# Performance work log

Hardware: AMD Instinct MI355X
Metric: run time of the kernel (lower is better)

Reference implementation:

```python
import jax, jax.numpy as jnp
import numpy as np

B, S, D, H = 32, 512, 1024, 16
DH = D // H
EPS = 1e-5
NEG = -1e9


def layer_norm(x, g, b):
    mu = jnp.mean(x, axis=-1, keepdims=True)
    var = jnp.mean(jnp.square(x - mu), axis=-1, keepdims=True)
    return (x - mu) * jax.lax.rsqrt(var + EPS) * g + b


def setup_inputs() -> dict:
    key = jax.random.key(0)
    ks = jax.random.split(key, 12)
    s = 1.0 / np.sqrt(D)
    inp = {
        "qk": jax.random.normal(ks[0], (B, S, D), jnp.float32),
        "v": jax.random.normal(ks[1], (B, S, D), jnp.float32),
        "mask": jax.random.randint(ks[2], (B, S), 0, 2).astype(jnp.int32),
        "qk_ln_g": jnp.ones((D,), jnp.float32),
        "qk_ln_b": jnp.zeros((D,), jnp.float32),
        "v_ln_g": jnp.ones((D,), jnp.float32),
        "v_ln_b": jnp.zeros((D,), jnp.float32),
        "Wq": jax.random.normal(ks[3], (D, D), jnp.float32) * s,
        "bq": jnp.zeros((D,), jnp.float32),
        "Wk": jax.random.normal(ks[4], (D, D), jnp.float32) * s,
        "bk": jnp.zeros((D,), jnp.float32),
        "Wv": jax.random.normal(ks[5], (D, D), jnp.float32) * s,
        "bv": jnp.zeros((D,), jnp.float32),
        "Wo": jax.random.normal(ks[6], (D, D), jnp.float32) * s,
        "bo": jnp.zeros((D,), jnp.float32),
    }
    return inp


def reference(qk, v, mask, qk_ln_g, qk_ln_b, v_ln_g, v_ln_b,
              Wq, bq, Wk, bk, Wv, bv, Wo, bo):
    # dual pre-norm
    qk_n = layer_norm(qk, qk_ln_g, qk_ln_b)          # [B,S,D]
    v_n = layer_norm(v, v_ln_g, v_ln_b)              # [B,S,D]
    # projections -> [B,S,H,DH]
    q = (qk_n @ Wq + bq).reshape(B, S, H, DH)
    k = (qk_n @ Wk + bk).reshape(B, S, H, DH)
    vv = (v_n @ Wv + bv).reshape(B, S, H, DH)
    # attention scores with key-padding mask
    scores = jnp.einsum("bqhd,bkhd->bhqk", q, k) / np.sqrt(DH)
    scores = jnp.where(mask[:, None, None, :] == 0, NEG, scores)
    attn = jax.nn.softmax(scores, axis=-1)           # [B,H,Sq,Sk]
    ctx = jnp.einsum("bhqk,bkhd->bqhd", attn, vv).reshape(B, S, D)
    a = ctx @ Wo + bo                                # output projection
    # residual on the normalized v (dropout is identity at eval)
    return v_n + a
```

## Files before the change

kernel.cpp:

```cpp
#include <hip/hip_runtime.h>
#include <hip/hip_bf16.h>

typedef __bf16 bf16;
typedef __bf16 bf16x2 __attribute__((ext_vector_type(2)));
typedef __bf16 bf16x4 __attribute__((ext_vector_type(4)));
typedef __bf16 bf16x8 __attribute__((ext_vector_type(8)));
typedef float f32x4 __attribute__((ext_vector_type(4)));

#define B_ 32
#define S_ 512
#define D_ 1024
#define H_ 16
#define DH_ 64
#define M_ (B_*S_)

#if __has_builtin(__builtin_amdgcn_exp2f)
#define FEXP2 __builtin_amdgcn_exp2f
#else
#define FEXP2 exp2f
#endif

__device__ __forceinline__ void async16(const void* g, void* l) {
  __builtin_amdgcn_global_load_lds(
      (const __attribute__((address_space(1))) unsigned int*)g,
      (__attribute__((address_space(3))) unsigned int*)l, 16, 0, 0);
}

__global__ __launch_bounds__(256) void ln_bf16(
    const float* __restrict__ qk, const float* __restrict__ v,
    const float* __restrict__ g1, const float* __restrict__ b1,
    const float* __restrict__ g2, const float* __restrict__ b2,
    bf16* __restrict__ o1, bf16* __restrict__ o2)
{
  int row = blockIdx.x;
  const float* src; const float* g; const float* b; bf16* o; int r;
  if (row < M_) { src=qk; g=g1; b=b1; o=o1; r=row; }
  else          { src=v;  g=g2; b=b2; o=o2; r=row-M_; }
  int t = threadIdx.x;
  float4 x = ((const float4*)(src + (size_t)r*D_))[t];
  float s  = x.x+x.y+x.z+x.w;
  float ss = x.x*x.x + x.y*x.y + x.z*x.z + x.w*x.w;
  #pragma unroll
  for (int off=32; off>=1; off>>=1) {
    s  += __shfl_xor(s,  off, 64);
    ss += __shfl_xor(ss, off, 64);
  }
  __shared__ float red[8];
  int w = t>>6, l = t&63;
  if (l==0){ red[w]=s; red[4+w]=ss; }
  __syncthreads();
  s  = red[0]+red[1]+red[2]+red[3];
  ss = red[4]+red[5]+red[6]+red[7];
  float mu  = s*(1.f/D_);
  float var = ss*(1.f/D_) - mu*mu;
  float rs  = rsqrtf(var + 1e-5f);
  float4 gg = ((const float4*)g)[t];
  float4 bb = ((const float4*)b)[t];
  bf16x4 ov;
  ov[0] = (bf16)((x.x-mu)*rs*gg.x + bb.x);
  ov[1] = (bf16)((x.y-mu)*rs*gg.y + bb.y);
  ov[2] = (bf16)((x.z-mu)*rs*gg.z + bb.z);
  ov[3] = (bf16)((x.w-mu)*rs*gg.w + bb.w);
  ((bf16x4*)(o + (size_t)r*D_))[t] = ov;
}

__global__ void wtrans(const float* __restrict__ W0, const float* __restrict__ W1,
                       const float* __restrict__ W2, const float* __restrict__ W3,
                       bf16* __restrict__ o0, bf16* __restrict__ o1,
                       bf16* __restrict__ o2, bf16* __restrict__ o3)
{
  int z = blockIdx.z;
  const float* W = z==0?W0: z==1?W1: z==2?W2: W3;
  bf16* o        = z==0?o0: z==1?o1: z==2?o2: o3;
  __shared__ float tile[32][33];
  int n0 = blockIdx.x*32, k0 = blockIdx.y*32;
  int tx = threadIdx.x, ty = threadIdx.y;
  #pragma unroll
  for (int i=0;i<4;i++) tile[ty + i*8][tx] = W[(size_t)(k0+ty+i*8)*D_ + n0+tx];
  __syncthreads();
  #pragma unroll
  for (int i=0;i<4;i++) o[(size_t)(n0+ty+i*8)*D_ + k0+tx] = (bf16)tile[tx][ty+i*8];
}

template<int MODE>
__global__ __launch_bounds__(512, 2) void gemm_bt(
    const bf16* __restrict__ A, const bf16* __restrict__ Bt,
    const float* __restrict__ bias0, const float* __restrict__ bias1,
    const bf16* __restrict__ res,
    bf16* __restrict__ out0, bf16* __restrict__ out1, float* __restrict__ outf)
{
  __shared__ bf16 A_sh[2][256*64];
  __shared__ bf16 B_sh[2][256*64];
  int t = threadIdx.x;
  int nwg  = gridDim.x * gridDim.y;
  int orig = blockIdx.y * gridDim.x + blockIdx.x;
  int qch  = nwg >> 3;
  int wg   = (orig & 7) * qch + (orig >> 3);
  int bx = wg % gridDim.x, by = wg / gridDim.x;
  int n0 = bx*256, m0 = by*256;
  int w = t>>6, l = t&63, lr = l&15, lg = (l>>4)&3;
  int wm = w>>2, wn = w&3;

  auto stage = [&](int buf, int kt){
    const bf16* Ab = A  + (size_t)m0*D_ + kt*64;
    const bf16* Bb = Bt + (size_t)n0*D_ + kt*64;
    #pragma unroll
    for (int i=0;i<4;i++){
      int c = i*512 + t;
      int row = c>>3, slot = (c&7) ^ (row&7);
      async16(Ab + (size_t)row*D_ + slot*8, &A_sh[buf][c*8]);
      async16(Bb + (size_t)row*D_ + slot*8, &B_sh[buf][c*8]);
    }
  };

  f32x4 acc[8][4];
  #pragma unroll
  for (int m=0;m<8;m++)
    #pragma unroll
    for (int n=0;n<4;n++) acc[m][n] = (f32x4){0.f,0.f,0.f,0.f};

  stage(0, 0);
  stage(1, 1);
  asm volatile("s_waitcnt vmcnt(8)" ::: "memory");
  __builtin_amdgcn_s_barrier();

  for (int kt=0; kt<16; ++kt) {
    int cur = kt & 1;
    bf16x8 bfr[4][2];
    #pragma unroll
    for (int n=0;n<4;n++){
      int row = wn*64 + n*16 + lr;
      #pragma unroll
      for (int kk=0;kk<2;kk++)
        bfr[n][kk] = *(const bf16x8*)&B_sh[cur][row*64 + (((kk*4+lg)^(lr&7))*8)];
    }
    __builtin_amdgcn_s_setprio(1);
    #pragma unroll
    for (int m=0;m<8;m++){
      int row = wm*128 + m*16 + lr;
      bf16x8 af0 = *(const bf16x8*)&A_sh[cur][row*64 + (((0*4+lg)^(lr&7))*8)];
      bf16x8 af1 = *(const bf16x8*)&A_sh[cur][row*64 + (((1*4+lg)^(lr&7))*8)];
      #pragma unroll
      for (int n=0;n<4;n++)
        acc[m][n] = __builtin_amdgcn_mfma_f32_16x16x32_bf16(af0, bfr[n][0], acc[m][n], 0,0,0);
      #pragma unroll
      for (int n=0;n<4;n++)
        acc[m][n] = __builtin_amdgcn_mfma_f32_16x16x32_bf16(af1, bfr[n][1], acc[m][n], 0,0,0);
    }
    __builtin_amdgcn_s_setprio(0);
    asm volatile("s_waitcnt lgkmcnt(0)" ::: "memory");
    __builtin_amdgcn_sched_barrier(0);
    __builtin_amdgcn_s_barrier();
    if (kt+2 < 16) stage(cur, kt+2);
    if (kt < 14)       asm volatile("s_waitcnt vmcnt(8)" ::: "memory");
    else if (kt == 14) asm volatile("s_waitcnt vmcnt(0)" ::: "memory");
    if (kt < 15) { __builtin_amdgcn_sched_barrier(0); __builtin_amdgcn_s_barrier(); }
  }

  if (MODE == 0) {
    #pragma unroll
    for (int n=0;n<4;n++){
      int col = n0 + wn*64 + n*16 + lr;
      bf16* dst; int c;
      if (col < D_) { dst = out0; c = col; } else { dst = out1; c = col - D_; }
      float bv = (col < D_) ? bias0[c] : bias1[c];
      #pragma unroll
      for (int m=0;m<8;m++){
        #pragma unroll
        for (int j=0;j<4;j++){
          size_t row = (size_t)m0 + wm*128 + m*16 + lg*4 + j;
          dst[row*D_ + c] = (bf16)(acc[m][n][j] + bv);
        }
      }
    }
  } else if (MODE == 1) {
    #pragma unroll
    for (int n=0;n<4;n++){
      int col = n0 + wn*64 + n*16 + lr;
      int hh = col >> 6, dh = col & 63;
      int nd = dh >> 4, lrk = dh & 15;
      float bv = bias0[col];
      #pragma unroll
      for (int m=0;m<8;m++){
        int row = m0 + wm*128 + m*16 + lg*4;
        int bb = row >> 9, sl = row & 511;
        int kt = sl >> 6, l0 = sl & 63;
        int kk = (l0>>5)&1, h8 = (l0>>4)&1, lgk = (l0>>2)&3;
        int c  = ((nd*2+kk)*4+lgk)*16 + lrk;
        bf16x4 pk4;
        #pragma unroll
        for (int j=0;j<4;j++) pk4[j] = (bf16)(acc[m][n][j] + bv);
        *(bf16x4*)&out0[(size_t)(((bb*H_ + hh)*8 + kt)*4096) + c*8 + h8*4] = pk4;
      }
    }
  } else {
    #pragma unroll
    for (int m=0;m<8;m++){
      #pragma unroll
      for (int j=0;j<4;j++){
        size_t row = (size_t)m0 + wm*128 + m*16 + lg*4 + j;
        #pragma unroll
        for (int n=0;n<4;n++){
          int col = n0 + wn*64 + n*16 + lr;
          size_t idx = row*D_ + col;
          outf[idx] = acc[m][n][j] + bias0[col] + (float)res[idx];
        }
      }
    }
  }
}

__global__ __launch_bounds__(512) void attn_fwd(
    const bf16* __restrict__ Q, const bf16* __restrict__ K,
    const bf16* __restrict__ VF, const int* __restrict__ mask,
    bf16* __restrict__ ctx)
{
  int flat = blockIdx.x + (blockIdx.y<<1) + (blockIdx.z<<5);
  int work = (flat & 7)*128 + (flat >> 3);
  int qt = work & 1, h = (work>>1) & 15, b = work >> 5;
  int q0 = qt*256;
  int t = threadIdx.x, w = t>>6, l = t&63, lr = l&15, lg = (l>>4)&3;

  __shared__ bf16 K_s[2][4096];
  __shared__ bf16 V_s[2][4096];
  __shared__ float msk[512];

  const float SC = 0.125f * 1.44269504f;
  msk[t] = mask[b*S_+t] ? 0.f : -1.44269504e9f;

  size_t qbase  = ((size_t)(b*S_ + q0)*H_ + h)*DH_;
  size_t vfbase = (size_t)(b*H_ + h)*8*4096;

  auto stageKV = [&](int slot, int kt){
    size_t kb = ((size_t)(b*S_ + kt*64)*H_ + h)*DH_;
    int clr=t&15, clg=(t>>4)&3, ckk=(t>>6)&1, n16=t>>7;
    async16(K + kb + (size_t)(n16*16+clr)*D_ + ckk*32 + clg*8, &K_s[slot][t*8]);
    async16(VF + vfbase + (size_t)kt*4096 + t*8, &V_s[slot][t*8]);
  };

  bf16x8 qa[2][2];
  #pragma unroll
  for (int s=0;s<2;s++)
    #pragma unroll
    for (int kk=0;kk<2;kk++)
      qa[s][kk] = *(const bf16x8*)(Q + qbase + (size_t)(w*32 + s*16 + lr)*D_ + kk*32 + lg*8);

  stageKV(0, 0);
  stageKV(1, 1);
  asm volatile("s_waitcnt vmcnt(2) lgkmcnt(0)" ::: "memory");
  __builtin_amdgcn_s_barrier();

  f32x4 cacc[2][4];
  #pragma unroll
  for (int s=0;s<2;s++)
    #pragma unroll
    for (int n=0;n<4;n++) cacc[s][n] = (f32x4){0.f,0.f,0.f,0.f};
  float mrun[2] = {-3.0e38f, -3.0e38f};
  float lrun[2] = {0.f, 0.f};

  union UPA { unsigned u[4]; bf16x8 v; };
  UPA pa[2][2];

  for (int kt=0; kt<8; ++kt) {
    int cur = kt & 1;
    const bf16* Ks = K_s[cur];
    const bf16* Vs = V_s[cur];

    bf16x8 kf[4][2];
    #pragma unroll
    for (int n=0;n<4;n++)
      #pragma unroll
      for (int kk=0;kk<2;kk++)
        kf[n][kk] = *(const bf16x8*)&Ks[(((n*2+kk)*4+lg)*16+lr)*8];

    #pragma unroll
    for (int s=0;s<2;s++){
      float p[4][4];
      #pragma unroll
      for (int n=0;n<4;n++){
        f32x4 sa = (f32x4){0.f,0.f,0.f,0.f};
        #pragma unroll
        for (int kk=0;kk<2;kk++)
          sa = __builtin_amdgcn_mfma_f32_16x16x32_bf16(kf[n][kk], qa[s][kk], sa, 0,0,0);
        float4 mk = *(const float4*)&msk[kt*64 + n*16 + lg*4];
        p[n][0] = sa[0]*SC + mk.x;
        p[n][1] = sa[1]*SC + mk.y;
        p[n][2] = sa[2]*SC + mk.z;
        p[n][3] = sa[3]*SC + mk.w;
      }

      float pm = fmaxf(fmaxf(p[0][0],p[0][1]),fmaxf(p[0][2],p[0][3]));
      #pragma unroll
      for (int n=1;n<4;n++)
        pm = fmaxf(pm, fmaxf(fmaxf(p[n][0],p[n][1]),fmaxf(p[n][2],p[n][3])));
      pm = fmaxf(pm, __shfl_xor(pm, 16, 64));
      pm = fmaxf(pm, __shfl_xor(pm, 32, 64));

      if (__any((int)(pm - mrun[s] > 8.f))) {
        float mnew  = fmaxf(mrun[s], pm);
        float alpha = FEXP2(mrun[s] - mnew);
        mrun[s] = mnew;
        lrun[s] *= alpha;
        #pragma unroll
        for (int n=0;n<4;n++) cacc[s][n] *= alpha;
      }
      float ps = 0.f;
      #pragma unroll
      for (int n=0;n<4;n++)
        #pragma unroll
        for (int j=0;j<4;j++){ p[n][j] = FEXP2(p[n][j] - mrun[s]); ps += p[n][j]; }
      ps += __shfl_xor(ps, 16, 64);
      ps += __shfl_xor(ps, 32, 64);
      lrun[s] += ps;

      unsigned pk[4][2];
      #pragma unroll
      for (int n=0;n<4;n++)
        #pragma unroll
        for (int i=0;i<2;i++){
          union { bf16x2 v; unsigned u; } u2;
          u2.v[0] = (bf16)p[n][2*i];
          u2.v[1] = (bf16)p[n][2*i+1];
          pk[n][i] = u2.u;
        }
      #pragma unroll
      for (int kk=0;kk<2;kk++){
        pa[s][kk].u[0] = pk[2*kk  ][0];
        pa[s][kk].u[1] = pk[2*kk  ][1];
        pa[s][kk].u[2] = pk[2*kk+1][0];
        pa[s][kk].u[3] = pk[2*kk+1][1];
      }
    }

    __builtin_amdgcn_s_setprio(1);
    #pragma unroll
    for (int nd=0;nd<4;nd++){
      bf16x8 vb0 = *(const bf16x8*)&Vs[(((nd*2+0)*4+lg)*16+lr)*8];
      bf16x8 vb1 = *(const bf16x8*)&Vs[(((nd*2+1)*4+lg)*16+lr)*8];
      #pragma unroll
      for (int s=0;s<2;s++){
        cacc[s][nd] = __builtin_amdgcn_mfma_f32_16x16x32_bf16(vb0, pa[s][0].v, cacc[s][nd], 0,0,0);
        cacc[s][nd] = __builtin_amdgcn_mfma_f32_16x16x32_bf16(vb1, pa[s][1].v, cacc[s][nd], 0,0,0);
      }
    }
    __builtin_amdgcn_s_setprio(0);

    asm volatile("s_waitcnt lgkmcnt(0)" ::: "memory");
    __builtin_amdgcn_sched_barrier(0);
    __builtin_amdgcn_s_barrier();
    if (kt+2 < 8) stageKV(cur, kt+2);

    if (kt < 6)       asm volatile("s_waitcnt vmcnt(2)" ::: "memory");
    else if (kt == 6) asm volatile("s_waitcnt vmcnt(0)" ::: "memory");
    if (kt < 7) { __builtin_amdgcn_sched_barrier(0); __builtin_amdgcn_s_barrier(); }
  }

  #pragma unroll
  for (int s=0;s<2;s++){
    float rl = 1.0f / lrun[s];
    size_t obase = qbase + (size_t)(w*32 + s*16 + lr)*D_;
    #pragma unroll
    for (int nd=0;nd<4;nd++){
      bf16x4 o4;
      #pragma unroll
      for (int j=0;j<4;j++) o4[j] = (bf16)(cacc[s][nd][j]*rl);
      *(bf16x4*)&ctx[obase + nd*16 + lg*4] = o4;
    }
  }
}

extern "C" void kernel_launch(void* const* d_in, const int* in_sizes, int n_in,
                              void* d_out, int out_size, void* d_ws, size_t ws_size,
                              hipStream_t stream)
{
  (void)in_sizes; (void)n_in; (void)out_size; (void)ws_size;
  const float* qk   = (const float*)d_in[0];
  const float* v    = (const float*)d_in[1];
  const int*   mask = (const int*)  d_in[2];
  const float* qk_g = (const float*)d_in[3];
  const float* qk_b = (const float*)d_in[4];
  const float* v_g  = (const float*)d_in[5];
  const float* v_b  = (const float*)d_in[6];
  const float* Wq   = (const float*)d_in[7];
  const float* bq   = (const float*)d_in[8];
  const float* Wk   = (const float*)d_in[9];
  const float* bk   = (const float*)d_in[10];
  const float* Wv   = (const float*)d_in[11];
  const float* bv   = (const float*)d_in[12];
  const float* Wo   = (const float*)d_in[13];
  const float* bo   = (const float*)d_in[14];
  float* out = (float*)d_out;

  char* ws = (char*)d_ws;
  size_t off = 0;
  auto alloc = [&](size_t bytes){ void* p = ws + off; off += (bytes + 255) & ~(size_t)255; return p; };
  bf16* qkn  = (bf16*)alloc((size_t)M_*D_*2);
  bf16* vn   = (bf16*)alloc((size_t)M_*D_*2);
  bf16* Qb   = (bf16*)alloc((size_t)M_*D_*2);
  bf16* Kb   = (bf16*)alloc((size_t)M_*D_*2);
  bf16* VFb  = (bf16*)alloc((size_t)M_*D_*2);
  bf16* Cb   = (bf16*)alloc((size_t)M_*D_*2);
  bf16* WqkT = (bf16*)alloc((size_t)2*D_*D_*2);
  bf16* WvT  = (bf16*)alloc((size_t)D_*D_*2);
  bf16* WoT  = (bf16*)alloc((size_t)D_*D_*2);

  ln_bf16<<<2*M_, 256, 0, stream>>>(qk, v, qk_g, qk_b, v_g, v_b, qkn, vn);
  wtrans<<<dim3(32,32,4), dim3(32,8), 0, stream>>>(Wq, Wk, Wv, Wo,
      WqkT, WqkT + (size_t)D_*D_, WvT, WoT);
  gemm_bt<0><<<dim3(8,64), 512, 0, stream>>>(qkn, WqkT, bq, bk, nullptr, Qb, Kb, nullptr);
  gemm_bt<1><<<dim3(4,64), 512, 0, stream>>>(vn,  WvT,  bv, nullptr, nullptr, VFb, nullptr, nullptr);
  attn_fwd<<<dim3(2, 16, 32), 512, 0, stream>>>(Qb, Kb, VFb, mask, Cb);
  gemm_bt<2><<<dim3(4,64), 512, 0, stream>>>(Cb, WoT, bo, nullptr, vn, nullptr, nullptr, out);
}
```

Measured before the change: 274.9 us.

## Interleave split A/B tile loads with MFMA phases in GEMM main loop

Restructures the bf16 GEMM main loop into four sub-phases per k-tile. Each phase issues a half-tile async load of A (next k-tile) or B (two k-tiles ahead) between fragment reads and MFMA bursts, with a barrier per phase, so global-to-LDS traffic is spread across the compute instead of issued in one burst. It also drops the occupancy hint of 2 blocks per CU from launch bounds, which frees registers but may lower occupancy. The extra barriers and the tighter buffer reuse add synchronisation overhead and risk of LDS races.

After: 259.9 us. 5.4% less time.

```diff
diff --git a/kernel.cpp b/kernel.cpp
--- a/kernel.cpp
+++ b/kernel.cpp
@@ -83,7 +83,7 @@
 }
 
 template<int MODE>
-__global__ __launch_bounds__(512, 2) void gemm_bt(
+__global__ __launch_bounds__(512) void gemm8(
     const bf16* __restrict__ A, const bf16* __restrict__ Bt,
     const float* __restrict__ bias0, const float* __restrict__ bias1,
     const bf16* __restrict__ res,
@@ -101,17 +101,28 @@
   int w = t>>6, l = t&63, lr = l&15, lg = (l>>4)&3;
   int wm = w>>2, wn = w&3;
 
-  auto stage = [&](int buf, int kt){
-    const bf16* Ab = A  + (size_t)m0*D_ + kt*64;
-    const bf16* Bb = Bt + (size_t)n0*D_ + kt*64;
-    #pragma unroll
-    for (int i=0;i<4;i++){
+  auto stageA = [&](int kt, int half){
+    if (kt >= 16) return;
+    int buf = kt & 1;
+    const bf16* Ab = A + (size_t)(m0 + half*128)*D_ + kt*64;
+    #pragma unroll
+    for (int i=0;i<2;i++){
       int c = i*512 + t;
       int row = c>>3, slot = (c&7) ^ (row&7);
-      async16(Ab + (size_t)row*D_ + slot*8, &A_sh[buf][c*8]);
-      async16(Bb + (size_t)row*D_ + slot*8, &B_sh[buf][c*8]);
+      async16(Ab + (size_t)row*D_ + slot*8, &A_sh[buf][(half*1024 + c)*8]);
     }
   };
+  auto stageB = [&](int kt, int half){
+    if (kt >= 16) return;
+    int buf = kt & 1;
+    const bf16* Bb = Bt + (size_t)(n0 + half*128)*D_ + kt*64;
+    #pragma unroll
+    for (int i=0;i<2;i++){
+      int c = i*512 + t;
+      int row = c>>3, slot = (c&7) ^ (row&7);
+      async16(Bb + (size_t)row*D_ + slot*8, &B_sh[buf][(half*1024 + c)*8]);
+    }
+  };
 
   f32x4 acc[8][4];
   #pragma unroll
@@ -119,42 +130,60 @@
     #pragma unroll
     for (int n=0;n<4;n++) acc[m][n] = (f32x4){0.f,0.f,0.f,0.f};
 
-  stage(0, 0);
-  stage(1, 1);
-  asm volatile("s_waitcnt vmcnt(8)" ::: "memory");
+  stageA(0,0); stageA(0,1); stageB(0,0); stageB(0,1);
+  stageB(1,0); stageB(1,1);
+  asm volatile("s_waitcnt vmcnt(4)" ::: "memory");
   __builtin_amdgcn_s_barrier();
 
-  for (int kt=0; kt<16; ++kt) {
-    int cur = kt & 1;
-    bf16x8 bfr[4][2];
-    #pragma unroll
-    for (int n=0;n<4;n++){
-      int row = wn*64 + n*16 + lr;
-      #pragma unroll
-      for (int kk=0;kk<2;kk++)
-        bfr[n][kk] = *(const bf16x8*)&B_sh[cur][row*64 + (((kk*4+lg)^(lr&7))*8)];
-    }
-    __builtin_amdgcn_s_setprio(1);
-    #pragma unroll
-    for (int m=0;m<8;m++){
-      int row = wm*128 + m*16 + lr;
-      bf16x8 af0 = *(const bf16x8*)&A_sh[cur][row*64 + (((0*4+lg)^(lr&7))*8)];
-      bf16x8 af1 = *(const bf16x8*)&A_sh[cur][row*64 + (((1*4+lg)^(lr&7))*8)];
-      #pragma unroll
-      for (int n=0;n<4;n++)
-        acc[m][n] = __builtin_amdgcn_mfma_f32_16x16x32_bf16(af0, bfr[n][0], acc[m][n], 0,0,0);
-      #pragma unroll
-      for (int n=0;n<4;n++)
-        acc[m][n] = __builtin_amdgcn_mfma_f32_16x16x32_bf16(af1, bfr[n][1], acc[m][n], 0,0,0);
-    }
-    __builtin_amdgcn_s_setprio(0);
-    asm volatile("s_waitcnt lgkmcnt(0)" ::: "memory");
-    __builtin_amdgcn_sched_barrier(0);
-    __builtin_amdgcn_s_barrier();
-    if (kt+2 < 16) stage(cur, kt+2);
-    if (kt < 14)       asm volatile("s_waitcnt vmcnt(8)" ::: "memory");
-    else if (kt == 14) asm volatile("s_waitcnt vmcnt(0)" ::: "memory");
-    if (kt < 15) { __builtin_amdgcn_sched_barrier(0); __builtin_amdgcn_s_barrier(); }
+  for (int pr=0; pr<8; ++pr) {
+    #pragma unroll
+    for (int half=0; half<2; ++half) {
+      int kt = pr*2 + half;
+      int buf = half;
+      bf16x8 bfr[4][2];
+      #pragma unroll
+      for (int mp=0; mp<4; ++mp) {
+        if (mp == 0) {
+          #pragma unroll
+          for (int n=0;n<4;n++){
+            int row = wn*64 + n*16 + lr;
+            #pragma unroll
+            for (int kk=0;kk<2;kk++)
+              bfr[n][kk] = *(const bf16x8*)&B_sh[buf][row*64 + (((kk*4+lg)^(lr&7))*8)];
+          }
+        }
+        bf16x8 af[2][2];
+        #pragma unroll
+        for (int i=0;i<2;i++){
+          int row = wm*128 + (mp*2+i)*16 + lr;
+          #pragma unroll
+          for (int kk=0;kk<2;kk++)
+            af[i][kk] = *(const bf16x8*)&A_sh[buf][row*64 + (((kk*4+lg)^(lr&7))*8)];
+        }
+        if      (mp == 0) stageA(kt+1, 0);
+        else if (mp == 1) stageA(kt+1, 1);
+        else if (mp == 2) stageB(kt+2, 0);
+        else              stageB(kt+2, 1);
+        __builtin_amdgcn_s_barrier();
+        asm volatile("s_waitcnt lgkmcnt(0)" ::: "memory");
+        __builtin_amdgcn_sched_barrier(0);
+        __builtin_amdgcn_s_setprio(1);
+        #pragma unroll
+        for (int kk=0;kk<2;kk++)
+          #pragma unroll
+          for (int i=0;i<2;i++)
+            #pragma unroll
+            for (int n=0;n<4;n++)
+              acc[mp*2+i][n] = __builtin_amdgcn_mfma_f32_16x16x32_bf16(
+                  af[i][kk], bfr[n][kk], acc[mp*2+i][n], 0,0,0);
+        __builtin_amdgcn_s_setprio(0);
+        if (mp == 3) {
+          if (pr == 7 && half == 0) asm volatile("s_waitcnt vmcnt(0)" ::: "memory");
+          else                      asm volatile("s_waitcnt vmcnt(4)" ::: "memory");
+        }
+        __builtin_amdgcn_s_barrier();
+      }
+    }
   }
 
   if (MODE == 0) {
@@ -407,8 +436,8 @@
   ln_bf16<<<2*M_, 256, 0, stream>>>(qk, v, qk_g, qk_b, v_g, v_b, qkn, vn);
   wtrans<<<dim3(32,32,4), dim3(32,8), 0, stream>>>(Wq, Wk, Wv, Wo,
       WqkT, WqkT + (size_t)D_*D_, WvT, WoT);
-  gemm_bt<0><<<dim3(8,64), 512, 0, stream>>>(qkn, WqkT, bq, bk, nullptr, Qb, Kb, nullptr);
-  gemm_bt<1><<<dim3(4,64), 512, 0, stream>>>(vn,  WvT,  bv, nullptr, nullptr, VFb, nullptr, nullptr);
+  gemm8<0><<<dim3(8,64), 512, 0, stream>>>(qkn, WqkT, bq, bk, nullptr, Qb, Kb, nullptr);
+  gemm8<1><<<dim3(4,64), 512, 0, stream>>>(vn,  WvT,  bv, nullptr, nullptr, VFb, nullptr, nullptr);
   attn_fwd<<<dim3(2, 16, 32), 512, 0, stream>>>(Qb, Kb, VFb, mask, Cb);
-  gemm_bt<2><<<dim3(4,64), 512, 0, stream>>>(Cb, WoT, bo, nullptr, vn, nullptr, nullptr, out);
-}
+  gemm8<2><<<dim3(4,64), 512, 0, stream>>>(Cb, WoT, bo, nullptr, vn, nullptr, nullptr, out);
+}
```
